# Kernel optimization log

Hardware: AMD Instinct MI355X
Metric: run time of the kernel (lower is better)

## Reference

```python
import jax, jax.numpy as jnp
import numpy as np

NMS_RADIUS = 4   # default_config['nms_radius']
MAX_KP = 256     # default_config['max_keypoints']


def _conv2d(x, w, b):
    y = jax.lax.conv_general_dilated(x, w, (1, 1), [(1, 1), (1, 1)],
                                     dimension_numbers=('NCHW', 'OIHW', 'NCHW'))
    return y + b[None, :, None, None]


def _conv1d(x, w, b, pad):
    y = jax.lax.conv_general_dilated(x, w, (1,), [(pad, pad)],
                                     dimension_numbers=('NCH', 'OIH', 'NCH'))
    return y + b[None, :, None]


def _maxpool(x, r):
    k = 2 * r + 1
    return jax.lax.reduce_window(x, -jnp.inf, jax.lax.max,
                                 (1, k, k), (1, 1, 1), [(0, 0), (r, r), (r, r)])


def _simple_nms(scores, r):
    zeros = jnp.zeros_like(scores)
    max_mask = scores == _maxpool(scores, r)
    for _ in range(2):
        supp_mask = _maxpool(max_mask.astype(scores.dtype), r) > 0
        supp_scores = jnp.where(supp_mask, zeros, scores)
        new_max_mask = supp_scores == _maxpool(supp_scores, r)
        max_mask = max_mask | (new_max_mask & ~supp_mask)
    return jnp.where(max_mask, scores, zeros)


def _affine_grid(theta, H, W):
    # F.affine_grid with align_corners=False
    xs = (jnp.arange(W, dtype=theta.dtype) + 0.5) * (2.0 / W) - 1.0
    ys = (jnp.arange(H, dtype=theta.dtype) + 0.5) * (2.0 / H) - 1.0
    Y, X = jnp.meshgrid(ys, xs, indexing='ij')  # (H, W)
    gx = theta[:, 0, 0, None, None] * X + theta[:, 0, 1, None, None] * Y + theta[:, 0, 2, None, None]
    gy = theta[:, 1, 0, None, None] * X + theta[:, 1, 1, None, None] * Y + theta[:, 1, 2, None, None]
    return jnp.stack([gx, gy], axis=-1)  # (N, H, W, 2)


def _grid_sample(img, grid):
    # F.grid_sample, bilinear, padding_mode='zeros', align_corners=False
    N, C, H, W = img.shape
    ix = ((grid[..., 0] + 1.0) * W - 1.0) * 0.5
    iy = ((grid[..., 1] + 1.0) * H - 1.0) * 0.5
    x0 = jnp.floor(ix); y0 = jnp.floor(iy)
    x1 = x0 + 1.0;      y1 = y0 + 1.0

    def gather(xi, yi):
        valid = (xi >= 0) & (xi <= W - 1) & (yi >= 0) & (yi <= H - 1)
        xc = jnp.clip(xi, 0, W - 1).astype(jnp.int32)
        yc = jnp.clip(yi, 0, H - 1).astype(jnp.int32)
        v = jax.vmap(lambda im, y, x: im[:, y, x])(img, yc, xc)  # (N, C, H, W)
        return v * valid[:, None].astype(img.dtype)

    wa = ((x1 - ix) * (y1 - iy))[:, None]
    wb = ((ix - x0) * (y1 - iy))[:, None]
    wc = ((x1 - ix) * (iy - y0))[:, None]
    wd = ((ix - x0) * (iy - y0))[:, None]
    return (gather(x0, y0) * wa + gather(x1, y0) * wb +
            gather(x0, y1) * wc + gather(x1, y1) * wd)


def setup_inputs() -> dict:
    key = jax.random.key(0)
    ks = jax.random.split(key, 12)
    L, C, H, W = 4, 256, 128, 256
    Cd = C // 2
    s = 0.02
    return {
        'feats':   jax.random.normal(ks[0], (L, C, H, W), jnp.float32),
        'convS_w': jax.random.normal(ks[1], (1, C, 3, 3), jnp.float32) * s,
        'convS_b': jax.random.normal(ks[2], (1,), jnp.float32) * s,
        'convD_w': jax.random.normal(ks[3], (Cd, C, 3, 3), jnp.float32) * s,
        'convD_b': jax.random.normal(ks[4], (Cd,), jnp.float32) * s,
        'proj_w':  jax.random.normal(ks[5], (Cd, Cd, 3), jnp.float32) * s,
        'proj_b':  jax.random.normal(ks[6], (Cd,), jnp.float32) * s,
        'projS_w': jax.random.normal(ks[7], (Cd, Cd, 1), jnp.float32) * s,
        'projS_b': jax.random.normal(ks[8], (Cd,), jnp.float32) * s,
        'final_w': jax.random.normal(ks[9], (3, Cd, 1), jnp.float32) * s,
        'final_b': jax.random.normal(ks[10], (3,), jnp.float32) * s,
    }


def reference(feats, convS_w, convS_b, convD_w, convD_b,
              proj_w, proj_b, projS_w, projS_b, final_w, final_b):
    L, C, H, W = feats.shape
    scores = jax.nn.sigmoid(_conv2d(feats, convS_w, convS_b))[:, 0]   # (L, H, W)
    desc = jax.nn.relu(_conv2d(feats, convD_w, convD_b))               # (L, C//2, H, W)

    scores = _simple_nms(scores, NMS_RADIUS).reshape(L, -1)
    _, top_idx = jax.lax.top_k(scores, MAX_KP)                         # (L, K)

    # F.normalize(p=2, dim=1)
    norm = jnp.sqrt(jnp.sum(desc * desc, axis=1, keepdims=True))
    desc = desc / jnp.maximum(norm, 1e-12)
    desc = desc.reshape(L, desc.shape[1], -1)                          # (L, Cd, HW)
    desc = jnp.take_along_axis(desc, top_idx[:, None, :], axis=2)      # (L, Cd, K)

    # AttentionalGNN: out = desc + (desc + message) = 2*desc + message
    Cd = desc.shape[1]
    qkv = jnp.transpose(desc, (2, 0, 1))                               # (K, L, Cd)
    attn = jnp.einsum('knc,kmc->knm', qkv, qkv) / jnp.sqrt(jnp.asarray(Cd, desc.dtype))
    prob = jax.nn.softmax(attn, axis=-1)
    message = jnp.einsum('knm,kmc->knc', prob, qkv)
    desc = 2.0 * desc + jnp.transpose(message, (1, 2, 0))

    desc = jax.nn.relu(_conv1d(desc, proj_w, proj_b, 1))
    s = _conv1d(desc, projS_w, projS_b, 0)
    order = jnp.argsort(-s, axis=-1)                                   # sort descending per channel
    desc = jnp.take_along_axis(desc, order, axis=-1)
    desc = _conv1d(desc, final_w, final_b, 0)                          # (L, 3, K)
    desc = desc - desc[0:1]

    idx = jnp.argmin(jnp.abs(desc), axis=2, keepdims=True)             # (L, 3, 1)
    picked = jnp.take_along_axis(desc, idx, axis=2)[:, :, 0]           # (L, 3)
    # picked * (picked/|picked|) == picked * sign(picked); sign(0)=0 matches the
    # original's nan->0 replacement for the first (zero-difference) sample.
    min_desc = picked * jnp.sign(picked)
    # the original builds t_matrix from Python floats (math.cos), detaching grads
    min_desc = jax.lax.stop_gradient(min_desc)

    th, tx, ty = min_desc[:, 2], min_desc[:, 0], min_desc[:, 1]
    row0 = jnp.stack([jnp.cos(th), -jnp.sin(th), tx], axis=1)
    row1 = jnp.stack([jnp.sin(th), jnp.cos(th), ty], axis=1)
    theta = jnp.stack([row0, row1], axis=1)                            # (L, 2, 3)

    grid = _affine_grid(theta, H, W)
    return _grid_sample(feats, grid)
```

## Files before the change

kernel.cpp:

```cpp
#include <hip/hip_runtime.h>

#define LIMG 4
#define CIN 256
#define HH 128
#define WW 256
#define HW 32768
#define LHW 131072
#define CD 128
#define KP 256
#define CAP 8192
#define NSP 2
#define CPER (CIN/NSP)
#define NINF -3.402823466e38f

__global__ void k_wtrans(const float* __restrict__ wD, float* __restrict__ wT,
                         int* __restrict__ cnt) {
  int i = blockIdx.x * 256 + threadIdx.x;
  if (i < LIMG) cnt[i] = 0;
  if (i >= CD * CIN * 9) return;
  int d = i & (CD - 1);
  int j = i >> 7;
  wT[i] = wD[d * (CIN * 9) + j];
}

__global__ __launch_bounds__(256) void k_chanred(const float* __restrict__ feats,
                                                 const float* __restrict__ wS,
                                                 float* __restrict__ g) {
  int gp   = (blockIdx.x & 511) * 256 + threadIdx.x;
  int half = blockIdx.x >> 9;
  int l  = gp >> 15;
  int pi = gp & (HW - 1);
  const float* f = feats + (size_t)(l * CIN + half * CPER) * HW + pi;
  const float* w = wS + half * CPER * 9;
  float a0=0,a1=0,a2=0,a3=0,a4=0,a5=0,a6=0,a7=0,a8=0;
  #pragma unroll 4
  for (int c = 0; c < CPER; ++c) {
    float v = f[(size_t)c * HW];
    const float* wc = w + c * 9;
    a0 = fmaf(wc[0], v, a0); a1 = fmaf(wc[1], v, a1); a2 = fmaf(wc[2], v, a2);
    a3 = fmaf(wc[3], v, a3); a4 = fmaf(wc[4], v, a4); a5 = fmaf(wc[5], v, a5);
    a6 = fmaf(wc[6], v, a6); a7 = fmaf(wc[7], v, a7); a8 = fmaf(wc[8], v, a8);
  }
  float* go = g + (size_t)(half * 9) * LHW + gp;
  go[0*(size_t)LHW]=a0; go[1*(size_t)LHW]=a1; go[2*(size_t)LHW]=a2;
  go[3*(size_t)LHW]=a3; go[4*(size_t)LHW]=a4; go[5*(size_t)LHW]=a5;
  go[6*(size_t)LHW]=a6; go[7*(size_t)LHW]=a7; go[8*(size_t)LHW]=a8;
}

__global__ __launch_bounds__(256) void k_scores(const float* __restrict__ g,
                                                const float* __restrict__ bS,
                                                float* __restrict__ scores) {
  int gp = blockIdx.x * 256 + threadIdx.x;
  int l  = gp >> 15;
  int pi = gp & (HW - 1);
  int y = pi >> 8, x = pi & 255;
  float acc = bS[0];
  #pragma unroll
  for (int ky = 0; ky < 3; ++ky) {
    int yy = y + ky - 1;
    if (yy < 0 || yy >= HH) continue;
    #pragma unroll
    for (int kx = 0; kx < 3; ++kx) {
      int xx = x + kx - 1;
      if (xx < 0 || xx >= WW) continue;
      int tap = ky * 3 + kx;
      size_t q = (size_t)l * HW + yy * WW + xx;
      acc += g[(size_t)tap * LHW + q] + g[(size_t)(9 + tap) * LHW + q];
    }
  }
  scores[gp] = 1.0f / (1.0f + expf(-acc));
}

#define PROWS 8
__global__ __launch_bounds__(256) void k_nms0(const float* __restrict__ scores,
                                              float* __restrict__ mask) {
  __shared__ float raw[PROWS + 8][WW];
  __shared__ float rm[PROWS + 8][WW];
  int b = blockIdx.x;
  int l = b >> 4;
  int y0 = (b & 15) * PROWS;
  int x = threadIdx.x;
  const float* inl = scores + (size_t)l * HW;
  #pragma unroll
  for (int r = 0; r < PROWS + 8; ++r) {
    int yy = y0 - 4 + r;
    raw[r][x] = (yy >= 0 && yy < HH) ? inl[yy * WW + x] : NINF;
  }
  __syncthreads();
  #pragma unroll
  for (int r = 0; r < PROWS + 8; ++r) {
    float m = NINF;
    #pragma unroll
    for (int dx = -4; dx <= 4; ++dx) {
      int xx = x + dx;
      if (xx >= 0 && xx < WW) m = fmaxf(m, raw[r][xx]);
    }
    rm[r][x] = m;
  }
  __syncthreads();
  #pragma unroll
  for (int r = 0; r < PROWS; ++r) {
    float m = NINF;
    #pragma unroll
    for (int t = 0; t < 9; ++t) m = fmaxf(m, rm[r + t][x]);
    mask[l * HW + (y0 + r) * WW + x] = (m == raw[r + 4][x]) ? 1.0f : 0.0f;
  }
}

__global__ __launch_bounds__(256) void k_nmspair(const float* __restrict__ maskin,
                                                 const float* __restrict__ scores,
                                                 float* __restrict__ maskout,
                                                 int collect,
                                                 int* __restrict__ cnt,
                                                 int* __restrict__ cidx,
                                                 float* __restrict__ csc) {
  __shared__ float m24[PROWS + 16][WW];
  __shared__ float rm[PROWS + 16][WW];
  __shared__ float ss[PROWS + 8][WW];
  __shared__ float rs[PROWS + 8][WW];
  __shared__ float smc[PROWS][WW];
  int b = blockIdx.x;
  int l = b >> 4;
  int y0 = (b & 15) * PROWS;
  int x = threadIdx.x;
  const float* ml = maskin + (size_t)l * HW;
  const float* sl = scores + (size_t)l * HW;
  #pragma unroll
  for (int r = 0; r < PROWS + 16; ++r) {
    int yy = y0 - 8 + r;
    m24[r][x] = (yy >= 0 && yy < HH) ? ml[yy * WW + x] : 0.0f;
  }
  __syncthreads();
  #pragma unroll
  for (int r = 0; r < PROWS + 16; ++r) {
    float m = 0.0f;
    #pragma unroll
    for (int dx = -4; dx <= 4; ++dx) {
      int xx = x + dx;
      if (xx >= 0 && xx < WW) m = fmaxf(m, m24[r][xx]);
    }
    rm[r][x] = m;
  }
  __syncthreads();
  #pragma unroll
  for (int r2 = 0; r2 < PROWS + 8; ++r2) {
    float m = 0.0f;
    #pragma unroll
    for (int t = 0; t < 9; ++t) m = fmaxf(m, rm[r2 + t][x]);
    bool sm = m > 0.0f;
    int yy = y0 - 4 + r2;
    float sv = (yy >= 0 && yy < HH) ? sl[yy * WW + x] : 0.0f;
    ss[r2][x] = sm ? 0.0f : sv;
    if (r2 >= 4 && r2 < 4 + PROWS) smc[r2 - 4][x] = sm ? 1.0f : 0.0f;
  }
  __syncthreads();
  #pragma unroll
  for (int r2 = 0; r2 < PROWS + 8; ++r2) {
    float m = NINF;
    #pragma unroll
    for (int dx = -4; dx <= 4; ++dx) {
      int xx = x + dx;
      if (xx >= 0 && xx < WW) m = fmaxf(m, ss[r2][xx]);
    }
    rs[r2][x] = m;
  }
  __syncthreads();
  #pragma unroll
  for (int r = 0; r < PROWS; ++r) {
    float m = NINF;
    #pragma unroll
    for (int t = 0; t < 9; ++t) m = fmaxf(m, rs[r + t][x]);
    bool nm = (ss[r + 4][x] == m) && (smc[r][x] == 0.0f);
    float prev = m24[r + 8][x];
    float outv = (prev != 0.0f || nm) ? 1.0f : 0.0f;
    int p = (y0 + r) * WW + x;
    maskout[l * HW + p] = outv;
    if (collect && outv != 0.0f) {
      int pos = atomicAdd(&cnt[l], 1);
      if (pos < CAP) {
        cidx[l * CAP + pos] = p;
        csc[l * CAP + pos]  = sl[p];
      }
    }
  }
}

__global__ __launch_bounds__(256) void k_rankfill(const int* __restrict__ cnt,
                                                  const int* __restrict__ cidx,
                                                  const float* __restrict__ csc,
                                                  const float* __restrict__ mask,
                                                  int* __restrict__ sel) {
  __shared__ unsigned long long keys[CAP];
  __shared__ int csum[256];
  int b = blockIdx.x;
  int l = b >> 3;
  int tid = threadIdx.x;
  int M = cnt[l]; if (M > CAP) M = CAP;
  const int* ci = cidx + l * CAP;
  const float* cs = csc + l * CAP;
  for (int j = tid; j < M; j += 256) {
    unsigned int ks = __float_as_uint(cs[j]);
    keys[j] = ((unsigned long long)(0xFFFFFFFFu - ks) << 32) | (unsigned int)ci[j];
  }
  __syncthreads();
  for (int i = (b & 7) * 256 + tid; i < M; i += 2048) {
    unsigned long long ki = keys[i];
    int rank = 0;
    for (int j = 0; j < M; ++j)
      rank += (keys[j] < ki) ? 1 : 0;
    if (rank < KP) sel[l * KP + rank] = (int)(unsigned int)(ki & 0xFFFFFFFFu);
  }
  if ((b & 7) != 0) return;
  int Mc = (M < KP) ? M : KP;
  int need = KP - Mc;
  if (need > 0) {
    const float* mk = mask + (size_t)l * HW;
    const int per = HW / 256;
    int base = tid * per;
    int c = 0;
    for (int q = 0; q < per; ++q) c += (mk[base + q] == 0.0f) ? 1 : 0;
    int inc = c;
    csum[tid] = c;
    __syncthreads();
    for (int s = 1; s < 256; s <<= 1) {
      int v = (tid >= s) ? csum[tid - s] : 0;
      __syncthreads();
      csum[tid] += v;
      __syncthreads();
    }
    int excl = csum[tid] - inc;
    if (excl < need) {
      int r = excl;
      for (int q = 0; q < per && r < need; ++q) {
        if (mk[base + q] == 0.0f) { sel[l * KP + Mc + r] = base + q; ++r; }
      }
    }
  }
}

__global__ __launch_bounds__(256) void k_desc1(const float* __restrict__ feats,
                                               const float* __restrict__ wT,
                                               const int* __restrict__ sel,
                                               float* __restrict__ pacc) {
  __shared__ float patch[16][576];
  __shared__ int kpix[16];
  int b = blockIdx.x;
  int q  = b & 3;
  int kb = (b >> 2) & 15;
  int l  = b >> 6;
  int k0 = kb * 16;
  int tid = threadIdx.x;
  if (tid < 16) kpix[tid] = sel[l * KP + k0 + tid];
  __syncthreads();
  int c0 = q * 64;
  for (int e = tid; e < 16 * 576; e += 256) {
    int kp = e / 576;
    int j  = e - kp * 576;
    int c  = j / 9;
    int tap = j - c * 9;
    int ky = tap / 3, kx = tap - ky * 3;
    int pix = kpix[kp];
    int y = pix >> 8, x = pix & 255;
    int yy = y + ky - 1, xx = x + kx - 1;
    float v = 0.0f;
    if (yy >= 0 && yy < HH && xx >= 0 && xx < WW)
      v = feats[((size_t)(l * CIN + c0 + c) * HH + yy) * WW + xx];
    patch[kp][j] = v;
  }
  __syncthreads();
  int d = tid & 127;
  int g = tid >> 7;
  const float* w = wT + (size_t)(q * 576) * CD + d;
  float a[8] = {0.f,0.f,0.f,0.f,0.f,0.f,0.f,0.f};
  #pragma unroll 2
  for (int j = 0; j < 576; j += 4) {
    float w0 = w[(size_t)(j + 0) * CD];
    float w1 = w[(size_t)(j + 1) * CD];
    float w2 = w[(size_t)(j + 2) * CD];
    float w3 = w[(size_t)(j + 3) * CD];
    #pragma unroll
    for (int i = 0; i < 8; ++i) {
      float4 qv = *(const float4*)&patch[8 * g + i][j];
      a[i] = fmaf(w0, qv.x, a[i]);
      a[i] = fmaf(w1, qv.y, a[i]);
      a[i] = fmaf(w2, qv.z, a[i]);
      a[i] = fmaf(w3, qv.w, a[i]);
    }
  }
  size_t base = (((size_t)q * LIMG + l) * KP + k0 + 8 * g) * CD + d;
  #pragma unroll
  for (int i = 0; i < 8; ++i)
    pacc[base + (size_t)i * CD] = a[i];
}

__global__ __launch_bounds__(128) void k_desc2attn(const float* __restrict__ pacc,
                                                   const float* __restrict__ bD,
                                                   float* __restrict__ d2) {
  __shared__ float ps[2][LIMG];
  __shared__ float qs[LIMG][CD];
  __shared__ float dm[16];
  int k = blockIdx.x;
  int d = threadIdx.x;
  float bv = bD[d];
  float r[LIMG];
  #pragma unroll
  for (int l = 0; l < LIMG; ++l) {
    float s = bv;
    #pragma unroll
    for (int qq = 0; qq < 4; ++qq)
      s += pacc[(((size_t)qq * LIMG + l) * KP + k) * CD + d];
    r[l] = fmaxf(s, 0.0f);
  }
  int lane = d & 63, wid = d >> 6;
  #pragma unroll
  for (int l = 0; l < LIMG; ++l) {
    float v = r[l] * r[l];
    #pragma unroll
    for (int sh = 32; sh > 0; sh >>= 1) v += __shfl_down(v, sh);
    if (lane == 0) ps[wid][l] = v;
  }
  __syncthreads();
  float q[LIMG];
  #pragma unroll
  for (int l = 0; l < LIMG; ++l) {
    float n = fmaxf(sqrtf(ps[0][l] + ps[1][l]), 1e-12f);
    q[l] = r[l] / n;
    qs[l][d] = q[l];
  }
  __syncthreads();
  if (d < 16) {
    int n = d >> 2, m = d & 3;
    float s = 0.f;
    for (int t = 0; t < CD; ++t) s = fmaf(qs[n][t], qs[m][t], s);
    dm[d] = s * 0.08838834764831843f;
  }
  __syncthreads();
  #pragma unroll
  for (int n = 0; n < LIMG; ++n) {
    float a0 = dm[n*4+0], a1 = dm[n*4+1], a2 = dm[n*4+2], a3 = dm[n*4+3];
    float mx = fmaxf(fmaxf(a0, a1), fmaxf(a2, a3));
    float e0 = expf(a0 - mx), e1 = expf(a1 - mx), e2 = expf(a2 - mx), e3 = expf(a3 - mx);
    float inv = 1.0f / (e0 + e1 + e2 + e3);
    float msg = (e0 * q[0] + e1 * q[1] + e2 * q[2] + e3 * q[3]) * inv;
    d2[(size_t)(n * CD + d) * KP + k] = 2.0f * q[n] + msg;
  }
}

__global__ __launch_bounds__(256) void k_proj(const float* __restrict__ d2, const float* __restrict__ pw,
                                              const float* __restrict__ pb, float* __restrict__ d3) {
  int b = blockIdx.x;
  int l = b >> 7, o = b & 127;
  int k = threadIdx.x;
  float acc = pb[o];
  for (int c = 0; c < CD; ++c) {
    const float* row = d2 + (size_t)(l * CD + c) * KP;
    float xm = (k > 0)      ? row[k - 1] : 0.f;
    float x0 = row[k];
    float xp = (k < KP - 1) ? row[k + 1] : 0.f;
    const float* w = pw + (size_t)(o * CD + c) * 3;
    acc = fmaf(w[0], xm, acc);
    acc = fmaf(w[1], x0, acc);
    acc = fmaf(w[2], xp, acc);
  }
  d3[(size_t)(l * CD + o) * KP + k] = fmaxf(acc, 0.f);
}

__global__ __launch_bounds__(256) void k_projsort(const float* __restrict__ d3,
                                                  const float* __restrict__ psw,
                                                  const float* __restrict__ psb,
                                                  float* __restrict__ d4) {
  int b = blockIdx.x;
  int l = b >> 7, o = b & 127;
  int k = threadIdx.x;
  __shared__ float srow[KP];
  float acc = psb[o];
  for (int c = 0; c < CD; ++c)
    acc = fmaf(psw[o * CD + c], d3[(size_t)(l * CD + c) * KP + k], acc);
  srow[k] = acc;
  __syncthreads();
  int rank = 0;
  for (int m = 0; m < KP; ++m) {
    float sm = srow[m];
    rank += (sm > acc || (sm == acc && m < k)) ? 1 : 0;
  }
  int base = (l * CD + o) * KP;
  d4[base + rank] = d3[base + k];
}

__global__ __launch_bounds__(1024) void k_finaltheta(const float* __restrict__ d4,
                                                     const float* __restrict__ fw,
                                                     const float* __restrict__ fb,
                                                     float* __restrict__ theta) {
  __shared__ float accs[LIMG][KP][3];
  __shared__ float res[LIMG][3];
  int tid = threadIdx.x;
  int l = tid >> 8, k = tid & 255;
  float a0 = fb[0], a1 = fb[1], a2 = fb[2];
  const float* dl = d4 + (size_t)l * CD * KP + k;
  for (int c = 0; c < CD; ++c) {
    float v = dl[(size_t)c * KP];
    a0 = fmaf(fw[0 * CD + c], v, a0);
    a1 = fmaf(fw[1 * CD + c], v, a1);
    a2 = fmaf(fw[2 * CD + c], v, a2);
  }
  accs[l][k][0] = a0; accs[l][k][1] = a1; accs[l][k][2] = a2;
  __syncthreads();
  int wid = tid >> 6, lane = tid & 63;
  if (wid < 12) {
    int rl = wid / 3, ro = wid - rl * 3;
    float m = 3.402823466e38f;
    #pragma unroll
    for (int t = 0; t < 4; ++t) {
      int kk = lane + 64 * t;
      m = fminf(m, fabsf(accs[rl][kk][ro] - accs[0][kk][ro]));
    }
    #pragma unroll
    for (int s = 32; s > 0; s >>= 1) m = fminf(m, __shfl_down(m, s));
    if (lane == 0) res[rl][ro] = m;
  }
  __syncthreads();
  if (tid == 0) {
    for (int l2 = 0; l2 < LIMG; ++l2) {
      float tx = res[l2][0], ty = res[l2][1], th = res[l2][2];
      float cth = cosf(th), sth = sinf(th);
      theta[l2*6+0] = cth;  theta[l2*6+1] = -sth; theta[l2*6+2] = tx;
      theta[l2*6+3] = sth;  theta[l2*6+4] = cth;  theta[l2*6+5] = ty;
    }
  }
}

__global__ __launch_bounds__(256) void k_sample(const float* __restrict__ feats,
                                                const float* __restrict__ theta,
                                                float* __restrict__ out) {
  int b = blockIdx.x;
  int pb = b & 127;
  int cg = (b >> 7) & 31;
  int l  = b >> 12;
  int pi = pb * 256 + threadIdx.x;
  int x = pi & 255, y = pi >> 8;
  const float* t = theta + l * 6;
  float X = (x + 0.5f) * (2.0f / WW) - 1.0f;
  float Y = (y + 0.5f) * (2.0f / HH) - 1.0f;
  float gx = t[0] * X + t[1] * Y + t[2];
  float gy = t[3] * X + t[4] * Y + t[5];
  float ix = ((gx + 1.0f) * WW - 1.0f) * 0.5f;
  float iy = ((gy + 1.0f) * HH - 1.0f) * 0.5f;
  float x0 = floorf(ix), y0 = floorf(iy);
  float x1 = x0 + 1.0f,  y1 = y0 + 1.0f;
  float wa = (x1 - ix) * (y1 - iy);
  float wb = (ix - x0) * (y1 - iy);
  float wc = (x1 - ix) * (iy - y0);
  float wd = (ix - x0) * (iy - y0);
  bool vx0 = (x0 >= 0.f) && (x0 <= (float)(WW-1));
  bool vx1 = (x1 >= 0.f) && (x1 <= (float)(WW-1));
  bool vy0 = (y0 >= 0.f) && (y0 <= (float)(HH-1));
  bool vy1 = (y1 >= 0.f) && (y1 <= (float)(HH-1));
  wa = (vx0 && vy0) ? wa : 0.f;
  wb = (vx1 && vy0) ? wb : 0.f;
  wc = (vx0 && vy1) ? wc : 0.f;
  wd = (vx1 && vy1) ? wd : 0.f;
  int xc0 = (int)fminf(fmaxf(x0, 0.f), (float)(WW-1));
  int xc1 = (int)fminf(fmaxf(x1, 0.f), (float)(WW-1));
  int yc0 = (int)fminf(fmaxf(y0, 0.f), (float)(HH-1));
  int yc1 = (int)fminf(fmaxf(y1, 0.f), (float)(HH-1));
  int o00 = yc0 * WW + xc0;
  int o10 = yc0 * WW + xc1;
  int o01 = yc1 * WW + xc0;
  int o11 = yc1 * WW + xc1;
  const float* img = feats + (size_t)(l * CIN + cg * 8) * HW;
  float* op = out + (size_t)(l * CIN + cg * 8) * HW + pi;
  #pragma unroll
  for (int i = 0; i < 8; ++i) {
    const float* im = img + (size_t)i * HW;
    float acc = im[o00] * wa + im[o10] * wb + im[o01] * wc + im[o11] * wd;
    op[(size_t)i * HW] = acc;
  }
}

extern "C" void kernel_launch(void* const* d_in, const int* in_sizes, int n_in,
                              void* d_out, int out_size, void* d_ws, size_t ws_size,
                              hipStream_t stream) {
  const float* feats = (const float*)d_in[0];
  const float* wS    = (const float*)d_in[1];
  const float* bS    = (const float*)d_in[2];
  const float* wD    = (const float*)d_in[3];
  const float* bD    = (const float*)d_in[4];
  const float* pw    = (const float*)d_in[5];
  const float* pb    = (const float*)d_in[6];
  const float* psw   = (const float*)d_in[7];
  const float* psb   = (const float*)d_in[8];
  const float* fw    = (const float*)d_in[9];
  const float* fb    = (const float*)d_in[10];
  float* out = (float*)d_out;

  char* base = (char*)d_ws;
  size_t off = 0;
  auto alloc = [&](size_t bytes) -> void* {
    void* p = base + off;
    off = (off + bytes + 255) & ~(size_t)255;
    return p;
  };
  float* g      = (float*)alloc((size_t)NSP * 9 * LHW * sizeof(float));
  float* scores = (float*)alloc((size_t)LHW * 4);
  float* maskA  = (float*)alloc((size_t)LHW * 4);
  float* maskB  = (float*)alloc((size_t)LHW * 4);
  float* d2     = (float*)alloc((size_t)LHW * 4);
  float* d3     = (float*)alloc((size_t)LHW * 4);
  float* d4     = (float*)alloc((size_t)LHW * 4);
  float* wT     = (float*)alloc((size_t)CIN * 9 * CD * 4);
  float* pacc   = (float*)alloc((size_t)4 * LIMG * KP * CD * 4);
  float* theta  = (float*)alloc(24 * 4);
  float* csc    = (float*)alloc((size_t)LIMG * CAP * 4);
  int*   cidx   = (int*)  alloc((size_t)LIMG * CAP * 4);
  int*   cnt    = (int*)  alloc(64);
  int*   sel    = (int*)  alloc((size_t)LIMG * KP * 4);

  k_wtrans<<<(CD * CIN * 9 + 255) / 256, 256, 0, stream>>>(wD, wT, cnt);
  k_chanred<<<NSP * 512, 256, 0, stream>>>(feats, wS, g);
  k_scores<<<512, 256, 0, stream>>>(g, bS, scores);
  k_nms0<<<64, 256, 0, stream>>>(scores, maskA);
  k_nmspair<<<64, 256, 0, stream>>>(maskA, scores, maskB, 0, cnt, cidx, csc);
  k_nmspair<<<64, 256, 0, stream>>>(maskB, scores, maskA, 1, cnt, cidx, csc);
  k_rankfill<<<32, 256, 0, stream>>>(cnt, cidx, csc, maskA, sel);
  k_desc1<<<256, 256, 0, stream>>>(feats, wT, sel, pacc);
  k_desc2attn<<<256, 128, 0, stream>>>(pacc, bD, d2);
  k_proj<<<512, 256, 0, stream>>>(d2, pw, pb, d3);
  k_projsort<<<512, 256, 0, stream>>>(d3, psw, psb, d4);
  k_finaltheta<<<1, 1024, 0, stream>>>(d4, fw, fb, theta);
  k_sample<<<16384, 256, 0, stream>>>(feats, theta, out);
}
```

Measured before the change: 266.0 us.

## Fuse weight transpose, score conv, and first NMS rounds; retile descriptor conv

Folds the weight-transpose and counter reset into extra blocks of the channel-reduction kernel. It also fuses the score convolution, the initial max-pool NMS and the first suppression round into one kernel that recomputes halo rows, which drops two launches and the intermediate mask round-trips. The descriptor conv is retiled to 32 keypoints × 32 channels per block with 16 accumulators per thread and 8 partial sums, so the downstream reduction now sums 8 partials. The cost is redundant halo recomputation in a low-occupancy 64-block kernel and higher register pressure.

```diff
diff --git a/kernel.cpp b/kernel.cpp
--- a/kernel.cpp
+++ b/kernel.cpp
@@ -13,21 +13,25 @@
 #define CPER (CIN/NSP)
 #define NINF -3.402823466e38f
 
-__global__ void k_wtrans(const float* __restrict__ wD, float* __restrict__ wT,
-                         int* __restrict__ cnt) {
-  int i = blockIdx.x * 256 + threadIdx.x;
-  if (i < LIMG) cnt[i] = 0;
-  if (i >= CD * CIN * 9) return;
-  int d = i & (CD - 1);
-  int j = i >> 7;
-  wT[i] = wD[d * (CIN * 9) + j];
-}
-
 __global__ __launch_bounds__(256) void k_chanred(const float* __restrict__ feats,
                                                  const float* __restrict__ wS,
-                                                 float* __restrict__ g) {
-  int gp   = (blockIdx.x & 511) * 256 + threadIdx.x;
-  int half = blockIdx.x >> 9;
+                                                 float* __restrict__ g,
+                                                 const float* __restrict__ wD,
+                                                 float* __restrict__ wT,
+                                                 int* __restrict__ cnt) {
+  int bid = blockIdx.x;
+  if (bid >= 1024) {
+    int i = (bid - 1024) * 256 + threadIdx.x;
+    if (i < LIMG) cnt[i] = 0;
+    if (i < CD * CIN * 9) {
+      int d = i & (CD - 1);
+      int j = i >> 7;
+      wT[i] = wD[d * (CIN * 9) + j];
+    }
+    return;
+  }
+  int gp   = (bid & 511) * 256 + threadIdx.x;
+  int half = bid >> 9;
   int l  = gp >> 15;
   int pi = gp & (HW - 1);
   const float* f = feats + (size_t)(l * CIN + half * CPER) * HW + pi;
@@ -47,73 +51,111 @@
   go[6*(size_t)LHW]=a6; go[7*(size_t)LHW]=a7; go[8*(size_t)LHW]=a8;
 }
 
-__global__ __launch_bounds__(256) void k_scores(const float* __restrict__ g,
-                                                const float* __restrict__ bS,
-                                                float* __restrict__ scores) {
-  int gp = blockIdx.x * 256 + threadIdx.x;
-  int l  = gp >> 15;
-  int pi = gp & (HW - 1);
-  int y = pi >> 8, x = pi & 255;
-  float acc = bS[0];
-  #pragma unroll
-  for (int ky = 0; ky < 3; ++ky) {
-    int yy = y + ky - 1;
-    if (yy < 0 || yy >= HH) continue;
-    #pragma unroll
-    for (int kx = 0; kx < 3; ++kx) {
-      int xx = x + kx - 1;
-      if (xx < 0 || xx >= WW) continue;
-      int tap = ky * 3 + kx;
-      size_t q = (size_t)l * HW + yy * WW + xx;
-      acc += g[(size_t)tap * LHW + q] + g[(size_t)(9 + tap) * LHW + q];
-    }
-  }
-  scores[gp] = 1.0f / (1.0f + expf(-acc));
-}
-
-#define PROWS 8
-__global__ __launch_bounds__(256) void k_nms0(const float* __restrict__ scores,
-                                              float* __restrict__ mask) {
-  __shared__ float raw[PROWS + 8][WW];
-  __shared__ float rm[PROWS + 8][WW];
+__global__ __launch_bounds__(256) void k_nmsA(const float* __restrict__ g,
+                                              const float* __restrict__ bS,
+                                              float* __restrict__ scores,
+                                              float* __restrict__ maskout) {
+  __shared__ float sS[32][WW];
+  __shared__ float sR[32][WW];
+  __shared__ float sM[24][WW];
+  __shared__ float ss[16][WW];
+  __shared__ float rs[16][WW];
   int b = blockIdx.x;
   int l = b >> 4;
-  int y0 = (b & 15) * PROWS;
+  int y0 = (b & 15) * 8;
   int x = threadIdx.x;
-  const float* inl = scores + (size_t)l * HW;
-  #pragma unroll
-  for (int r = 0; r < PROWS + 8; ++r) {
-    int yy = y0 - 4 + r;
-    raw[r][x] = (yy >= 0 && yy < HH) ? inl[yy * WW + x] : NINF;
-  }
-  __syncthreads();
-  #pragma unroll
-  for (int r = 0; r < PROWS + 8; ++r) {
+  float bias = bS[0];
+  for (int r = 0; r < 32; ++r) {
+    int y = y0 - 12 + r;
+    float v = NINF;
+    if (y >= 0 && y < HH) {
+      float acc = bias;
+      #pragma unroll
+      for (int ky = 0; ky < 3; ++ky) {
+        int yy = y + ky - 1;
+        if (yy < 0 || yy >= HH) continue;
+        #pragma unroll
+        for (int kx = 0; kx < 3; ++kx) {
+          int xx = x + kx - 1;
+          if (xx < 0 || xx >= WW) continue;
+          int tap = ky * 3 + kx;
+          size_t qof = (size_t)l * HW + yy * WW + xx;
+          acc += g[(size_t)tap * LHW + qof] + g[(size_t)(9 + tap) * LHW + qof];
+        }
+      }
+      v = 1.0f / (1.0f + expf(-acc));
+      if (y >= y0 && y < y0 + 8) scores[l * HW + y * WW + x] = v;
+    }
+    sS[r][x] = v;
+  }
+  __syncthreads();
+  for (int r = 0; r < 32; ++r) {
     float m = NINF;
     #pragma unroll
     for (int dx = -4; dx <= 4; ++dx) {
       int xx = x + dx;
-      if (xx >= 0 && xx < WW) m = fmaxf(m, raw[r][xx]);
-    }
-    rm[r][x] = m;
-  }
-  __syncthreads();
-  #pragma unroll
-  for (int r = 0; r < PROWS; ++r) {
+      if (xx >= 0 && xx < WW) m = fmaxf(m, sS[r][xx]);
+    }
+    sR[r][x] = m;
+  }
+  __syncthreads();
+  for (int r = 0; r < 24; ++r) {
+    int y = y0 - 8 + r;
     float m = NINF;
     #pragma unroll
-    for (int t = 0; t < 9; ++t) m = fmaxf(m, rm[r + t][x]);
-    mask[l * HW + (y0 + r) * WW + x] = (m == raw[r + 4][x]) ? 1.0f : 0.0f;
-  }
-}
-
-__global__ __launch_bounds__(256) void k_nmspair(const float* __restrict__ maskin,
-                                                 const float* __restrict__ scores,
-                                                 float* __restrict__ maskout,
-                                                 int collect,
-                                                 int* __restrict__ cnt,
-                                                 int* __restrict__ cidx,
-                                                 float* __restrict__ csc) {
+    for (int t = 0; t < 9; ++t) m = fmaxf(m, sR[r + t][x]);
+    sM[r][x] = (y >= 0 && y < HH && sS[r + 4][x] == m) ? 1.0f : 0.0f;
+  }
+  __syncthreads();
+  for (int r = 0; r < 24; ++r) {
+    float m = 0.0f;
+    #pragma unroll
+    for (int dx = -4; dx <= 4; ++dx) {
+      int xx = x + dx;
+      if (xx >= 0 && xx < WW) m = fmaxf(m, sM[r][xx]);
+    }
+    sR[r][x] = m;
+  }
+  __syncthreads();
+  float smcreg[8];
+  for (int r2 = 0; r2 < 16; ++r2) {
+    float m = 0.0f;
+    #pragma unroll
+    for (int t = 0; t < 9; ++t) m = fmaxf(m, sR[r2 + t][x]);
+    bool sm = m > 0.0f;
+    int y = y0 - 4 + r2;
+    float sv = (y >= 0 && y < HH) ? sS[r2 + 8][x] : 0.0f;
+    ss[r2][x] = sm ? 0.0f : sv;
+    if (r2 >= 4 && r2 < 12) smcreg[r2 - 4] = sm ? 1.0f : 0.0f;
+  }
+  __syncthreads();
+  for (int r2 = 0; r2 < 16; ++r2) {
+    float m = NINF;
+    #pragma unroll
+    for (int dx = -4; dx <= 4; ++dx) {
+      int xx = x + dx;
+      if (xx >= 0 && xx < WW) m = fmaxf(m, ss[r2][xx]);
+    }
+    rs[r2][x] = m;
+  }
+  __syncthreads();
+  for (int r = 0; r < 8; ++r) {
+    float m = NINF;
+    #pragma unroll
+    for (int t = 0; t < 9; ++t) m = fmaxf(m, rs[r + t][x]);
+    bool nm = (ss[r + 4][x] == m) && (smcreg[r] == 0.0f);
+    float prev = sM[r + 8][x];
+    maskout[l * HW + (y0 + r) * WW + x] = (prev != 0.0f || nm) ? 1.0f : 0.0f;
+  }
+}
+
+#define PROWS 8
+__global__ __launch_bounds__(256) void k_nmsB(const float* __restrict__ maskin,
+                                              const float* __restrict__ scores,
+                                              float* __restrict__ maskout,
+                                              int* __restrict__ cnt,
+                                              int* __restrict__ cidx,
+                                              float* __restrict__ csc) {
   __shared__ float m24[PROWS + 16][WW];
   __shared__ float rm[PROWS + 16][WW];
   __shared__ float ss[PROWS + 8][WW];
@@ -175,7 +217,7 @@
     float outv = (prev != 0.0f || nm) ? 1.0f : 0.0f;
     int p = (y0 + r) * WW + x;
     maskout[l * HW + p] = outv;
-    if (collect && outv != 0.0f) {
+    if (outv != 0.0f) {
       int pos = atomicAdd(&cnt[l], 1);
       if (pos < CAP) {
         cidx[l * CAP + pos] = p;
@@ -242,20 +284,20 @@
                                                const float* __restrict__ wT,
                                                const int* __restrict__ sel,
                                                float* __restrict__ pacc) {
-  __shared__ float patch[16][576];
-  __shared__ int kpix[16];
-  int b = blockIdx.x;
-  int q  = b & 3;
-  int kb = (b >> 2) & 15;
+  __shared__ float patch[32][288];
+  __shared__ int kpix[32];
+  int b = blockIdx.x;
+  int q  = b & 7;
+  int kb = (b >> 3) & 7;
   int l  = b >> 6;
-  int k0 = kb * 16;
+  int k0 = kb * 32;
   int tid = threadIdx.x;
-  if (tid < 16) kpix[tid] = sel[l * KP + k0 + tid];
-  __syncthreads();
-  int c0 = q * 64;
-  for (int e = tid; e < 16 * 576; e += 256) {
-    int kp = e / 576;
-    int j  = e - kp * 576;
+  if (tid < 32) kpix[tid] = sel[l * KP + k0 + tid];
+  __syncthreads();
+  int c0 = q * 32;
+  for (int e = tid; e < 32 * 288; e += 256) {
+    int kp = e / 288;
+    int j  = e - kp * 288;
     int c  = j / 9;
     int tap = j - c * 9;
     int ky = tap / 3, kx = tap - ky * 3;
@@ -269,27 +311,29 @@
   }
   __syncthreads();
   int d = tid & 127;
-  int g = tid >> 7;
-  const float* w = wT + (size_t)(q * 576) * CD + d;
-  float a[8] = {0.f,0.f,0.f,0.f,0.f,0.f,0.f,0.f};
+  int gg = tid >> 7;
+  const float* w = wT + (size_t)(q * 288) * CD + d;
+  float a[16];
+  #pragma unroll
+  for (int i = 0; i < 16; ++i) a[i] = 0.0f;
   #pragma unroll 2
-  for (int j = 0; j < 576; j += 4) {
+  for (int j = 0; j < 288; j += 4) {
     float w0 = w[(size_t)(j + 0) * CD];
     float w1 = w[(size_t)(j + 1) * CD];
     float w2 = w[(size_t)(j + 2) * CD];
     float w3 = w[(size_t)(j + 3) * CD];
     #pragma unroll
-    for (int i = 0; i < 8; ++i) {
-      float4 qv = *(const float4*)&patch[8 * g + i][j];
+    for (int i = 0; i < 16; ++i) {
+      float4 qv = *(const float4*)&patch[16 * gg + i][j];
       a[i] = fmaf(w0, qv.x, a[i]);
       a[i] = fmaf(w1, qv.y, a[i]);
       a[i] = fmaf(w2, qv.z, a[i]);
       a[i] = fmaf(w3, qv.w, a[i]);
     }
   }
-  size_t base = (((size_t)q * LIMG + l) * KP + k0 + 8 * g) * CD + d;
-  #pragma unroll
-  for (int i = 0; i < 8; ++i)
+  size_t base = (((size_t)q * LIMG + l) * KP + k0 + 16 * gg) * CD + d;
+  #pragma unroll
+  for (int i = 0; i < 16; ++i)
     pacc[base + (size_t)i * CD] = a[i];
 }
 
@@ -307,7 +351,7 @@
   for (int l = 0; l < LIMG; ++l) {
     float s = bv;
     #pragma unroll
-    for (int qq = 0; qq < 4; ++qq)
+    for (int qq = 0; qq < 8; ++qq)
       s += pacc[(((size_t)qq * LIMG + l) * KP + k) * CD + d];
     r[l] = fmaxf(s, 0.0f);
   }
@@ -508,20 +552,18 @@
   float* d3     = (float*)alloc((size_t)LHW * 4);
   float* d4     = (float*)alloc((size_t)LHW * 4);
   float* wT     = (float*)alloc((size_t)CIN * 9 * CD * 4);
-  float* pacc   = (float*)alloc((size_t)4 * LIMG * KP * CD * 4);
+  float* pacc   = (float*)alloc((size_t)8 * LIMG * KP * CD * 4);
   float* theta  = (float*)alloc(24 * 4);
   float* csc    = (float*)alloc((size_t)LIMG * CAP * 4);
   int*   cidx   = (int*)  alloc((size_t)LIMG * CAP * 4);
   int*   cnt    = (int*)  alloc(64);
   int*   sel    = (int*)  alloc((size_t)LIMG * KP * 4);
 
-  k_wtrans<<<(CD * CIN * 9 + 255) / 256, 256, 0, stream>>>(wD, wT, cnt);
-  k_chanred<<<NSP * 512, 256, 0, stream>>>(feats, wS, g);
-  k_scores<<<512, 256, 0, stream>>>(g, bS, scores);
-  k_nms0<<<64, 256, 0, stream>>>(scores, maskA);
-  k_nmspair<<<64, 256, 0, stream>>>(maskA, scores, maskB, 0, cnt, cidx, csc);
-  k_nmspair<<<64, 256, 0, stream>>>(maskB, scores, maskA, 1, cnt, cidx, csc);
-  k_rankfill<<<32, 256, 0, stream>>>(cnt, cidx, csc, maskA, sel);
+  const int WT_BLOCKS = (CD * CIN * 9 + 255) / 256;
+  k_chanred<<<1024 + WT_BLOCKS, 256, 0, stream>>>(feats, wS, g, wD, wT, cnt);
+  k_nmsA<<<64, 256, 0, stream>>>(g, bS, scores, maskA);
+  k_nmsB<<<64, 256, 0, stream>>>(maskA, scores, maskB, cnt, cidx, csc);
+  k_rankfill<<<32, 256, 0, stream>>>(cnt, cidx, csc, maskB, sel);
   k_desc1<<<256, 256, 0, stream>>>(feats, wT, sel, pacc);
   k_desc2attn<<<256, 128, 0, stream>>>(pacc, bD, d2);
   k_proj<<<512, 256, 0, stream>>>(d2, pw, pb, d3);
```

After: 359.2 us. 1.35x slower.

## Fold weight transpose into chanred launch and retile desc1 to 32 keypoints

Applied to the files above, without the earlier changes.

The separate weight-transpose kernel is merged into the channel-reduction launch as extra blocks, removing one kernel launch and letting the two pieces of work run concurrently. The desc1 kernel is retiled so each block handles 32 keypoints over 32 channels (8 channel splits) instead of 16 keypoints over 64 channels, doubling weight reuse per load from global memory. Each thread now holds 16 accumulators, which raises register pressure. The partial-sum buffer doubles in size, so desc2attn has to reduce 8 partials instead of 4.

```diff
diff --git a/kernel.cpp b/kernel.cpp
--- a/kernel.cpp
+++ b/kernel.cpp
@@ -13,21 +13,25 @@
 #define CPER (CIN/NSP)
 #define NINF -3.402823466e38f
 
-__global__ void k_wtrans(const float* __restrict__ wD, float* __restrict__ wT,
-                         int* __restrict__ cnt) {
-  int i = blockIdx.x * 256 + threadIdx.x;
-  if (i < LIMG) cnt[i] = 0;
-  if (i >= CD * CIN * 9) return;
-  int d = i & (CD - 1);
-  int j = i >> 7;
-  wT[i] = wD[d * (CIN * 9) + j];
-}
-
 __global__ __launch_bounds__(256) void k_chanred(const float* __restrict__ feats,
                                                  const float* __restrict__ wS,
-                                                 float* __restrict__ g) {
-  int gp   = (blockIdx.x & 511) * 256 + threadIdx.x;
-  int half = blockIdx.x >> 9;
+                                                 float* __restrict__ g,
+                                                 const float* __restrict__ wD,
+                                                 float* __restrict__ wT,
+                                                 int* __restrict__ cnt) {
+  int bid = blockIdx.x;
+  if (bid >= 1024) {
+    int i = (bid - 1024) * 256 + threadIdx.x;
+    if (i < LIMG) cnt[i] = 0;
+    if (i < CD * CIN * 9) {
+      int d = i & (CD - 1);
+      int j = i >> 7;
+      wT[i] = wD[d * (CIN * 9) + j];
+    }
+    return;
+  }
+  int gp   = (bid & 511) * 256 + threadIdx.x;
+  int half = bid >> 9;
   int l  = gp >> 15;
   int pi = gp & (HW - 1);
   const float* f = feats + (size_t)(l * CIN + half * CPER) * HW + pi;
@@ -242,20 +246,20 @@
                                                const float* __restrict__ wT,
                                                const int* __restrict__ sel,
                                                float* __restrict__ pacc) {
-  __shared__ float patch[16][576];
-  __shared__ int kpix[16];
-  int b = blockIdx.x;
-  int q  = b & 3;
-  int kb = (b >> 2) & 15;
+  __shared__ float patch[32][288];
+  __shared__ int kpix[32];
+  int b = blockIdx.x;
+  int q  = b & 7;
+  int kb = (b >> 3) & 7;
   int l  = b >> 6;
-  int k0 = kb * 16;
+  int k0 = kb * 32;
   int tid = threadIdx.x;
-  if (tid < 16) kpix[tid] = sel[l * KP + k0 + tid];
-  __syncthreads();
-  int c0 = q * 64;
-  for (int e = tid; e < 16 * 576; e += 256) {
-    int kp = e / 576;
-    int j  = e - kp * 576;
+  if (tid < 32) kpix[tid] = sel[l * KP + k0 + tid];
+  __syncthreads();
+  int c0 = q * 32;
+  for (int e = tid; e < 32 * 288; e += 256) {
+    int kp = e / 288;
+    int j  = e - kp * 288;
     int c  = j / 9;
     int tap = j - c * 9;
     int ky = tap / 3, kx = tap - ky * 3;
@@ -269,27 +273,29 @@
   }
   __syncthreads();
   int d = tid & 127;
-  int g = tid >> 7;
-  const float* w = wT + (size_t)(q * 576) * CD + d;
-  float a[8] = {0.f,0.f,0.f,0.f,0.f,0.f,0.f,0.f};
+  int gg = tid >> 7;
+  const float* w = wT + (size_t)(q * 288) * CD + d;
+  float a[16];
+  #pragma unroll
+  for (int i = 0; i < 16; ++i) a[i] = 0.0f;
   #pragma unroll 2
-  for (int j = 0; j < 576; j += 4) {
+  for (int j = 0; j < 288; j += 4) {
     float w0 = w[(size_t)(j + 0) * CD];
     float w1 = w[(size_t)(j + 1) * CD];
     float w2 = w[(size_t)(j + 2) * CD];
     float w3 = w[(size_t)(j + 3) * CD];
     #pragma unroll
-    for (int i = 0; i < 8; ++i) {
-      float4 qv = *(const float4*)&patch[8 * g + i][j];
+    for (int i = 0; i < 16; ++i) {
+      float4 qv = *(const float4*)&patch[16 * gg + i][j];
       a[i] = fmaf(w0, qv.x, a[i]);
       a[i] = fmaf(w1, qv.y, a[i]);
       a[i] = fmaf(w2, qv.z, a[i]);
       a[i] = fmaf(w3, qv.w, a[i]);
     }
   }
-  size_t base = (((size_t)q * LIMG + l) * KP + k0 + 8 * g) * CD + d;
-  #pragma unroll
-  for (int i = 0; i < 8; ++i)
+  size_t base = (((size_t)q * LIMG + l) * KP + k0 + 16 * gg) * CD + d;
+  #pragma unroll
+  for (int i = 0; i < 16; ++i)
     pacc[base + (size_t)i * CD] = a[i];
 }
 
@@ -307,7 +313,7 @@
   for (int l = 0; l < LIMG; ++l) {
     float s = bv;
     #pragma unroll
-    for (int qq = 0; qq < 4; ++qq)
+    for (int qq = 0; qq < 8; ++qq)
       s += pacc[(((size_t)qq * LIMG + l) * KP + k) * CD + d];
     r[l] = fmaxf(s, 0.0f);
   }
@@ -508,15 +514,15 @@
   float* d3     = (float*)alloc((size_t)LHW * 4);
   float* d4     = (float*)alloc((size_t)LHW * 4);
   float* wT     = (float*)alloc((size_t)CIN * 9 * CD * 4);
-  float* pacc   = (float*)alloc((size_t)4 * LIMG * KP * CD * 4);
+  float* pacc   = (float*)alloc((size_t)8 * LIMG * KP * CD * 4);
   float* theta  = (float*)alloc(24 * 4);
   float* csc    = (float*)alloc((size_t)LIMG * CAP * 4);
   int*   cidx   = (int*)  alloc((size_t)LIMG * CAP * 4);
   int*   cnt    = (int*)  alloc(64);
   int*   sel    = (int*)  alloc((size_t)LIMG * KP * 4);
 
-  k_wtrans<<<(CD * CIN * 9 + 255) / 256, 256, 0, stream>>>(wD, wT, cnt);
-  k_chanred<<<NSP * 512, 256, 0, stream>>>(feats, wS, g);
+  const int WT_BLOCKS = (CD * CIN * 9 + 255) / 256;
+  k_chanred<<<1024 + WT_BLOCKS, 256, 0, stream>>>(feats, wS, g, wD, wT, cnt);
   k_scores<<<512, 256, 0, stream>>>(g, bS, scores);
   k_nms0<<<64, 256, 0, stream>>>(scores, maskA);
   k_nmspair<<<64, 256, 0, stream>>>(maskA, scores, maskB, 0, cnt, cidx, csc);
```

Measured after the change: 278.3 us. +4.6%, slower.

## Fuse NMS stages with haloed 2D tiles and merge weight transpose into chanred

Applied to the files above, without the earlier changes.

Merges the initial max-mask NMS stage and the first suppression iteration into one kernel that works on 8x128 tiles with recomputed halos. The grid doubles from 64 to 128 blocks, which removes one launch and one global mask round trip. The weight-transpose and counter-reset work now runs as extra blocks of the channel-reduction kernel, removing another launch. The cost is redundant halo computation and idle threads in the narrower stages of each tile.

```diff
diff --git a/kernel.cpp b/kernel.cpp
--- a/kernel.cpp
+++ b/kernel.cpp
@@ -13,21 +13,25 @@
 #define CPER (CIN/NSP)
 #define NINF -3.402823466e38f
 
-__global__ void k_wtrans(const float* __restrict__ wD, float* __restrict__ wT,
-                         int* __restrict__ cnt) {
-  int i = blockIdx.x * 256 + threadIdx.x;
-  if (i < LIMG) cnt[i] = 0;
-  if (i >= CD * CIN * 9) return;
-  int d = i & (CD - 1);
-  int j = i >> 7;
-  wT[i] = wD[d * (CIN * 9) + j];
-}
-
 __global__ __launch_bounds__(256) void k_chanred(const float* __restrict__ feats,
                                                  const float* __restrict__ wS,
-                                                 float* __restrict__ g) {
-  int gp   = (blockIdx.x & 511) * 256 + threadIdx.x;
-  int half = blockIdx.x >> 9;
+                                                 float* __restrict__ g,
+                                                 const float* __restrict__ wD,
+                                                 float* __restrict__ wT,
+                                                 int* __restrict__ cnt) {
+  int bid = blockIdx.x;
+  if (bid >= 1024) {
+    int i = (bid - 1024) * 256 + threadIdx.x;
+    if (i < LIMG) cnt[i] = 0;
+    if (i < CD * CIN * 9) {
+      int d = i & (CD - 1);
+      int j = i >> 7;
+      wT[i] = wD[d * (CIN * 9) + j];
+    }
+    return;
+  }
+  int gp   = (bid & 511) * 256 + threadIdx.x;
+  int half = bid >> 9;
   int l  = gp >> 15;
   int pi = gp & (HW - 1);
   const float* f = feats + (size_t)(l * CIN + half * CPER) * HW + pi;
@@ -71,115 +75,177 @@
   scores[gp] = 1.0f / (1.0f + expf(-acc));
 }
 
-#define PROWS 8
-__global__ __launch_bounds__(256) void k_nms0(const float* __restrict__ scores,
-                                              float* __restrict__ mask) {
-  __shared__ float raw[PROWS + 8][WW];
-  __shared__ float rm[PROWS + 8][WW];
-  int b = blockIdx.x;
-  int l = b >> 4;
-  int y0 = (b & 15) * PROWS;
-  int x = threadIdx.x;
-  const float* inl = scores + (size_t)l * HW;
-  #pragma unroll
-  for (int r = 0; r < PROWS + 8; ++r) {
-    int yy = y0 - 4 + r;
-    raw[r][x] = (yy >= 0 && yy < HH) ? inl[yy * WW + x] : NINF;
-  }
-  __syncthreads();
-  #pragma unroll
-  for (int r = 0; r < PROWS + 8; ++r) {
-    float m = NINF;
-    #pragma unroll
-    for (int dx = -4; dx <= 4; ++dx) {
-      int xx = x + dx;
-      if (xx >= 0 && xx < WW) m = fmaxf(m, raw[r][xx]);
-    }
-    rm[r][x] = m;
-  }
-  __syncthreads();
-  #pragma unroll
-  for (int r = 0; r < PROWS; ++r) {
-    float m = NINF;
-    #pragma unroll
-    for (int t = 0; t < 9; ++t) m = fmaxf(m, rm[r + t][x]);
-    mask[l * HW + (y0 + r) * WW + x] = (m == raw[r + 4][x]) ? 1.0f : 0.0f;
-  }
-}
-
-__global__ __launch_bounds__(256) void k_nmspair(const float* __restrict__ maskin,
-                                                 const float* __restrict__ scores,
-                                                 float* __restrict__ maskout,
-                                                 int collect,
-                                                 int* __restrict__ cnt,
-                                                 int* __restrict__ cidx,
-                                                 float* __restrict__ csc) {
-  __shared__ float m24[PROWS + 16][WW];
-  __shared__ float rm[PROWS + 16][WW];
-  __shared__ float ss[PROWS + 8][WW];
-  __shared__ float rs[PROWS + 8][WW];
-  __shared__ float smc[PROWS][WW];
-  int b = blockIdx.x;
-  int l = b >> 4;
-  int y0 = (b & 15) * PROWS;
-  int x = threadIdx.x;
+__global__ __launch_bounds__(256) void k_nms01(const float* __restrict__ scores,
+                                               float* __restrict__ maskout) {
+  __shared__ float sS[32][152];
+  __shared__ float buf[32][152];
+  __shared__ float sM[24][144];
+  __shared__ float ss[16][136];
+  __shared__ float smc[8][128];
+  int b = blockIdx.x;
+  int l  = b >> 5;
+  int yt = (b >> 1) & 15;
+  int xt = b & 1;
+  int y0 = yt * 8;
+  int x0 = xt * 128;
+  int tid = threadIdx.x;
+  const float* sl = scores + (size_t)l * HW;
+  if (tid < 152) {
+    int gx = x0 - 12 + tid;
+    bool vx = (gx >= 0 && gx < WW);
+    for (int r = 0; r < 32; ++r) {
+      int gy = y0 - 12 + r;
+      sS[r][tid] = (vx && gy >= 0 && gy < HH) ? sl[gy * WW + gx] : NINF;
+    }
+  }
+  __syncthreads();
+  if (tid < 144) {
+    for (int r = 0; r < 32; ++r) {
+      float m = sS[r][tid];
+      #pragma unroll
+      for (int dx = 1; dx <= 8; ++dx) m = fmaxf(m, sS[r][tid + dx]);
+      buf[r][tid] = m;
+    }
+  }
+  __syncthreads();
+  if (tid < 144) {
+    int gx = x0 - 8 + tid;
+    bool vx = (gx >= 0 && gx < WW);
+    for (int r3 = 0; r3 < 24; ++r3) {
+      int gy = y0 - 8 + r3;
+      float m = buf[r3][tid];
+      #pragma unroll
+      for (int t = 1; t < 9; ++t) m = fmaxf(m, buf[r3 + t][tid]);
+      sM[r3][tid] = (vx && gy >= 0 && gy < HH && sS[r3 + 4][tid + 4] == m) ? 1.0f : 0.0f;
+    }
+  }
+  __syncthreads();
+  if (tid < 136) {
+    for (int r3 = 0; r3 < 24; ++r3) {
+      float m = sM[r3][tid];
+      #pragma unroll
+      for (int dx = 1; dx <= 8; ++dx) m = fmaxf(m, sM[r3][tid + dx]);
+      buf[r3][tid] = m;
+    }
+  }
+  __syncthreads();
+  if (tid < 136) {
+    int gx = x0 - 4 + tid;
+    bool vx = (gx >= 0 && gx < WW);
+    for (int r2 = 0; r2 < 16; ++r2) {
+      int gy = y0 - 4 + r2;
+      float m = buf[r2][tid];
+      #pragma unroll
+      for (int t = 1; t < 9; ++t) m = fmaxf(m, buf[r2 + t][tid]);
+      bool sm = m > 0.0f;
+      bool vin = vx && gy >= 0 && gy < HH;
+      ss[r2][tid] = (sm || !vin) ? 0.0f : sS[r2 + 8][tid + 8];
+      if (r2 >= 4 && r2 < 12 && tid >= 4 && tid < 132)
+        smc[r2 - 4][tid - 4] = sm ? 1.0f : 0.0f;
+    }
+  }
+  __syncthreads();
+  if (tid < 128) {
+    for (int r2 = 0; r2 < 16; ++r2) {
+      float m = ss[r2][tid];
+      #pragma unroll
+      for (int dx = 1; dx <= 8; ++dx) m = fmaxf(m, ss[r2][tid + dx]);
+      buf[r2][tid] = m;
+    }
+  }
+  __syncthreads();
+  if (tid < 128) {
+    int gx = x0 + tid;
+    for (int r = 0; r < 8; ++r) {
+      float m = buf[r][tid];
+      #pragma unroll
+      for (int t = 1; t < 9; ++t) m = fmaxf(m, buf[r + t][tid]);
+      bool nm = (ss[r + 4][tid + 4] == m) && (smc[r][tid] == 0.0f);
+      float prev = sM[r + 8][tid + 8];
+      maskout[l * HW + (y0 + r) * WW + gx] = (prev != 0.0f || nm) ? 1.0f : 0.0f;
+    }
+  }
+}
+
+__global__ __launch_bounds__(256) void k_nms2(const float* __restrict__ maskin,
+                                              const float* __restrict__ scores,
+                                              float* __restrict__ maskout,
+                                              int* __restrict__ cnt,
+                                              int* __restrict__ cidx,
+                                              float* __restrict__ csc) {
+  __shared__ float m24[24][144];
+  __shared__ float buf[24][144];
+  __shared__ float ss[16][136];
+  __shared__ float smc[8][128];
+  int b = blockIdx.x;
+  int l  = b >> 5;
+  int yt = (b >> 1) & 15;
+  int xt = b & 1;
+  int y0 = yt * 8;
+  int x0 = xt * 128;
+  int tid = threadIdx.x;
   const float* ml = maskin + (size_t)l * HW;
   const float* sl = scores + (size_t)l * HW;
-  #pragma unroll
-  for (int r = 0; r < PROWS + 16; ++r) {
-    int yy = y0 - 8 + r;
-    m24[r][x] = (yy >= 0 && yy < HH) ? ml[yy * WW + x] : 0.0f;
-  }
-  __syncthreads();
-  #pragma unroll
-  for (int r = 0; r < PROWS + 16; ++r) {
-    float m = 0.0f;
-    #pragma unroll
-    for (int dx = -4; dx <= 4; ++dx) {
-      int xx = x + dx;
-      if (xx >= 0 && xx < WW) m = fmaxf(m, m24[r][xx]);
-    }
-    rm[r][x] = m;
-  }
-  __syncthreads();
-  #pragma unroll
-  for (int r2 = 0; r2 < PROWS + 8; ++r2) {
-    float m = 0.0f;
-    #pragma unroll
-    for (int t = 0; t < 9; ++t) m = fmaxf(m, rm[r2 + t][x]);
-    bool sm = m > 0.0f;
-    int yy = y0 - 4 + r2;
-    float sv = (yy >= 0 && yy < HH) ? sl[yy * WW + x] : 0.0f;
-    ss[r2][x] = sm ? 0.0f : sv;
-    if (r2 >= 4 && r2 < 4 + PROWS) smc[r2 - 4][x] = sm ? 1.0f : 0.0f;
-  }
-  __syncthreads();
-  #pragma unroll
-  for (int r2 = 0; r2 < PROWS + 8; ++r2) {
-    float m = NINF;
-    #pragma unroll
-    for (int dx = -4; dx <= 4; ++dx) {
-      int xx = x + dx;
-      if (xx >= 0 && xx < WW) m = fmaxf(m, ss[r2][xx]);
-    }
-    rs[r2][x] = m;
-  }
-  __syncthreads();
-  #pragma unroll
-  for (int r = 0; r < PROWS; ++r) {
-    float m = NINF;
-    #pragma unroll
-    for (int t = 0; t < 9; ++t) m = fmaxf(m, rs[r + t][x]);
-    bool nm = (ss[r + 4][x] == m) && (smc[r][x] == 0.0f);
-    float prev = m24[r + 8][x];
-    float outv = (prev != 0.0f || nm) ? 1.0f : 0.0f;
-    int p = (y0 + r) * WW + x;
-    maskout[l * HW + p] = outv;
-    if (collect && outv != 0.0f) {
-      int pos = atomicAdd(&cnt[l], 1);
-      if (pos < CAP) {
-        cidx[l * CAP + pos] = p;
-        csc[l * CAP + pos]  = sl[p];
+  if (tid < 144) {
+    int gx = x0 - 8 + tid;
+    bool vx = (gx >= 0 && gx < WW);
+    for (int r = 0; r < 24; ++r) {
+      int gy = y0 - 8 + r;
+      m24[r][tid] = (vx && gy >= 0 && gy < HH) ? ml[gy * WW + gx] : 0.0f;
+    }
+  }
+  __syncthreads();
+  if (tid < 136) {
+    for (int r = 0; r < 24; ++r) {
+      float m = m24[r][tid];
+      #pragma unroll
+      for (int dx = 1; dx <= 8; ++dx) m = fmaxf(m, m24[r][tid + dx]);
+      buf[r][tid] = m;
+    }
+  }
+  __syncthreads();
+  if (tid < 136) {
+    int gx = x0 - 4 + tid;
+    bool vx = (gx >= 0 && gx < WW);
+    for (int r2 = 0; r2 < 16; ++r2) {
+      int gy = y0 - 4 + r2;
+      float m = buf[r2][tid];
+      #pragma unroll
+      for (int t = 1; t < 9; ++t) m = fmaxf(m, buf[r2 + t][tid]);
+      bool sm = m > 0.0f;
+      bool vin = vx && gy >= 0 && gy < HH;
+      ss[r2][tid] = (sm || !vin) ? 0.0f : sl[gy * WW + gx];
+      if (r2 >= 4 && r2 < 12 && tid >= 4 && tid < 132)
+        smc[r2 - 4][tid - 4] = sm ? 1.0f : 0.0f;
+    }
+  }
+  __syncthreads();
+  if (tid < 128) {
+    for (int r2 = 0; r2 < 16; ++r2) {
+      float m = ss[r2][tid];
+      #pragma unroll
+      for (int dx = 1; dx <= 8; ++dx) m = fmaxf(m, ss[r2][tid + dx]);
+      buf[r2][tid] = m;
+    }
+  }
+  __syncthreads();
+  if (tid < 128) {
+    int gx = x0 + tid;
+    for (int r = 0; r < 8; ++r) {
+      float m = buf[r][tid];
+      #pragma unroll
+      for (int t = 1; t < 9; ++t) m = fmaxf(m, buf[r + t][tid]);
+      bool nm = (ss[r + 4][tid + 4] == m) && (smc[r][tid] == 0.0f);
+      float prev = m24[r + 8][tid + 8];
+      float outv = (prev != 0.0f || nm) ? 1.0f : 0.0f;
+      int p = (y0 + r) * WW + gx;
+      maskout[l * HW + p] = outv;
+      if (outv != 0.0f) {
+        int pos = atomicAdd(&cnt[l], 1);
+        if (pos < CAP) {
+          cidx[l * CAP + pos] = p;
+          csc[l * CAP + pos]  = sl[p];
+        }
       }
     }
   }
@@ -269,7 +335,7 @@
   }
   __syncthreads();
   int d = tid & 127;
-  int g = tid >> 7;
+  int gg = tid >> 7;
   const float* w = wT + (size_t)(q * 576) * CD + d;
   float a[8] = {0.f,0.f,0.f,0.f,0.f,0.f,0.f,0.f};
   #pragma unroll 2
@@ -280,14 +346,14 @@
     float w3 = w[(size_t)(j + 3) * CD];
     #pragma unroll
     for (int i = 0; i < 8; ++i) {
-      float4 qv = *(const float4*)&patch[8 * g + i][j];
+      float4 qv = *(const float4*)&patch[8 * gg + i][j];
       a[i] = fmaf(w0, qv.x, a[i]);
       a[i] = fmaf(w1, qv.y, a[i]);
       a[i] = fmaf(w2, qv.z, a[i]);
       a[i] = fmaf(w3, qv.w, a[i]);
     }
   }
-  size_t base = (((size_t)q * LIMG + l) * KP + k0 + 8 * g) * CD + d;
+  size_t base = (((size_t)q * LIMG + l) * KP + k0 + 8 * gg) * CD + d;
   #pragma unroll
   for (int i = 0; i < 8; ++i)
     pacc[base + (size_t)i * CD] = a[i];
@@ -515,13 +581,12 @@
   int*   cnt    = (int*)  alloc(64);
   int*   sel    = (int*)  alloc((size_t)LIMG * KP * 4);
 
-  k_wtrans<<<(CD * CIN * 9 + 255) / 256, 256, 0, stream>>>(wD, wT, cnt);
-  k_chanred<<<NSP * 512, 256, 0, stream>>>(feats, wS, g);
+  const int WT_BLOCKS = (CD * CIN * 9 + 255) / 256;
+  k_chanred<<<1024 + WT_BLOCKS, 256, 0, stream>>>(feats, wS, g, wD, wT, cnt);
   k_scores<<<512, 256, 0, stream>>>(g, bS, scores);
-  k_nms0<<<64, 256, 0, stream>>>(scores, maskA);
-  k_nmspair<<<64, 256, 0, stream>>>(maskA, scores, maskB, 0, cnt, cidx, csc);
-  k_nmspair<<<64, 256, 0, stream>>>(maskB, scores, maskA, 1, cnt, cidx, csc);
-  k_rankfill<<<32, 256, 0, stream>>>(cnt, cidx, csc, maskA, sel);
+  k_nms01<<<128, 256, 0, stream>>>(scores, maskA);
+  k_nms2<<<128, 256, 0, stream>>>(maskA, scores, maskB, cnt, cidx, csc);
+  k_rankfill<<<32, 256, 0, stream>>>(cnt, cidx, csc, maskB, sel);
   k_desc1<<<256, 256, 0, stream>>>(feats, wT, sel, pacc);
   k_desc2attn<<<256, 128, 0, stream>>>(pacc, bD, d2);
   k_proj<<<512, 256, 0, stream>>>(d2, pw, pb, d3);
```

After: 235.3 us. -11.5%, faster.
